# Optimization experiments

Hardware: AMD Instinct MI355X
Metric: run time of the kernel (lower is better)

The kernel has to match this reference:

```python
import jax, jax.numpy as jnp
import numpy as np

B, P, D, A = 256, 196, 512, 512

def setup_inputs() -> dict:
    key = jax.random.key(0)
    ks = jax.random.split(key, 12)
    sc = 1.0 / np.sqrt(D)
    sa = 1.0 / np.sqrt(A)
    return {
        "encoder_out": jax.random.normal(ks[0], (B, P, D), jnp.float32),
        "decoder_hidden": jax.random.normal(ks[1], (B, D), jnp.float32),
        "st": jax.random.normal(ks[2], (B, D), jnp.float32),
        "Wv": jax.random.normal(ks[3], (D, A), jnp.float32) * sc,
        "bv": jnp.zeros((A,), jnp.float32),
        "Wh": jax.random.normal(ks[4], (D, A), jnp.float32) * sc,
        "bh": jnp.zeros((A,), jnp.float32),
        "Ws": jax.random.normal(ks[5], (D, A), jnp.float32) * sc,
        "bs": jnp.zeros((A,), jnp.float32),
        "Wav": jax.random.normal(ks[6], (A,), jnp.float32) * sa,
        "bav": jnp.zeros((), jnp.float32),
        "Was": jax.random.normal(ks[7], (A,), jnp.float32) * sa,
        "bas": jnp.zeros((), jnp.float32),
    }

def reference(encoder_out, decoder_hidden, st, Wv, bv, Wh, bh, Ws, bs, Wav, bav, Was, bas):
    # hidden: (B, A)
    hidden = decoder_hidden @ Wh + bh
    # v: (B, P, A)
    v = jnp.einsum('bpd,da->bpa', encoder_out, Wv) + bv
    # z_t: (B, P) -- additive attention scores over pixels
    z_t = jnp.einsum('bpa,a->bp', jnp.tanh(v + hidden[:, None, :]), Wav) + bav
    alpha_t = jax.nn.softmax(z_t, axis=1)
    # c_t: (B, D) -- attention-weighted encoding
    c_t = jnp.einsum('bpd,bp->bd', encoder_out, alpha_t)
    # sentinel branch: s (B, A), s_att (B, 1)
    s = st @ Ws + bs
    s_att = jnp.tanh(s + hidden) @ Was + bas  # (B,)
    z_t_extended = jnp.concatenate([z_t, s_att[:, None]], axis=1)  # (B, P+1)
    alpha_t_hat = jax.nn.softmax(z_t_extended, axis=1)
    beta_t = alpha_t_hat[:, -1:]  # (B, 1)
    c_hat_t = beta_t * st + (1.0 - beta_t) * c_t
    return (c_hat_t, alpha_t, beta_t)
```

## Files before the change

### kernel.cpp

```cpp
#include <hip/hip_runtime.h>
#include <hip/hip_bf16.h>
#include <cstdint>

#define B_ 256
#define P_ 196
#define D_ 512
#define A_ 512

#define OUT_CHAT  0
#define OUT_ALPHA (B_*D_)
#define OUT_BETA  (B_*D_ + B_*P_)

typedef unsigned short ushort_t;
typedef uint32_t u32;
typedef uint64_t u64;
typedef __attribute__((ext_vector_type(8))) __bf16 bf16x8;
typedef __attribute__((ext_vector_type(4))) float f32x4;

__device__ __forceinline__ ushort_t f2bf(float f) {
    union { float f; u32 i; } v; v.f = f;
    u32 r = (v.i + 0x7fffu + ((v.i >> 16) & 1u)) >> 16;
    return (ushort_t)r;
}
__device__ __forceinline__ float bfbits2f(u32 lo16) {
    union { u32 i; float f; } v; v.i = lo16 << 16; return v.f;
}
__device__ __forceinline__ u32 cvt2bf(float x, float y) {
    union { __hip_bfloat162 h; u32 u; } v;
    v.h = __float22bfloat162_rn(make_float2(x, y));
    return v.u;
}
__device__ __forceinline__ float tanh_fast(float x) {
    float e = __expf(2.0f * x);
    return 1.0f - 2.0f / (e + 1.0f);
}
__device__ __forceinline__ void async_load16(const ushort_t* g, ushort_t* l) {
    __builtin_amdgcn_global_load_lds(
        (const __attribute__((address_space(1))) unsigned int*)g,
        (__attribute__((address_space(3))) unsigned int*)l, 16, 0, 0);
}
__device__ __forceinline__ void fma8(float ap, uint4 v, float ac[8]) {
    ac[0] = fmaf(ap, bfbits2f(v.x & 0xffffu), ac[0]);
    ac[1] = fmaf(ap, bfbits2f(v.x >> 16),     ac[1]);
    ac[2] = fmaf(ap, bfbits2f(v.y & 0xffffu), ac[2]);
    ac[3] = fmaf(ap, bfbits2f(v.y >> 16),     ac[3]);
    ac[4] = fmaf(ap, bfbits2f(v.z & 0xffffu), ac[4]);
    ac[5] = fmaf(ap, bfbits2f(v.z >> 16),     ac[5]);
    ac[6] = fmaf(ap, bfbits2f(v.w & 0xffffu), ac[6]);
    ac[7] = fmaf(ap, bfbits2f(v.w >> 16),     ac[7]);
}

__global__ __launch_bounds__(256) void k_prep(
    const float* __restrict__ E, const float* __restrict__ dh,
    const float* __restrict__ st,
    const float* __restrict__ Wv, const float* __restrict__ Wh,
    const float* __restrict__ Ws,
    ushort_t* __restrict__ Ebf, ushort_t* __restrict__ dhbf,
    ushort_t* __restrict__ stbf,
    ushort_t* __restrict__ WvT, ushort_t* __restrict__ WhT,
    ushort_t* __restrict__ WsT)
{
    __shared__ ushort_t tile[32][33];
    int bx = blockIdx.x;
    if (bx < 12544) {
        size_t i0 = (size_t)bx * 512 + threadIdx.x;
        const float4* src = (const float4*)E;
        u64* dst = (u64*)Ebf;
        float4 v0 = src[i0];
        float4 v1 = src[i0 + 256];
        dst[i0]       = (u64)cvt2bf(v0.x, v0.y) | ((u64)cvt2bf(v0.z, v0.w) << 32);
        dst[i0 + 256] = (u64)cvt2bf(v1.x, v1.y) | ((u64)cvt2bf(v1.z, v1.w) << 32);
    } else if (bx < 12672) {
        int gid = (bx - 12544) * 256 + threadIdx.x;
        float4 dv = ((const float4*)dh)[gid];
        float4 sv = ((const float4*)st)[gid];
        ((u64*)dhbf)[gid] = (u64)cvt2bf(dv.x, dv.y) | ((u64)cvt2bf(dv.z, dv.w) << 32);
        ((u64*)stbf)[gid] = (u64)cvt2bf(sv.x, sv.y) | ((u64)cvt2bf(sv.z, sv.w) << 32);
    } else {
        int idx = bx - 12672;
        int z   = idx >> 8;
        int rem = idx & 255;
        int tby = rem >> 4, tbx = rem & 15;
        const float* W  = (z == 0) ? Wv  : (z == 1) ? Wh  : Ws;
        ushort_t*    WT = (z == 0) ? WvT : (z == 1) ? WhT : WsT;
        int t = threadIdx.x, r = t >> 5, c = t & 31;
#pragma unroll
        for (int i = 0; i < 4; ++i) {
            int row = r + 8 * i;
            tile[row][c] = f2bf(W[(size_t)(tby * 32 + row) * A_ + tbx * 32 + c]);
        }
        __syncthreads();
#pragma unroll
        for (int i = 0; i < 4; ++i) {
            int row = r + 8 * i;
            WT[(size_t)(tbx * 32 + row) * D_ + tby * 32 + c] = tile[c][row];
        }
    }
}

#define PADK 72

__global__ __launch_bounds__(256) void k1_mfma(
    const ushort_t* __restrict__ dhbf, const ushort_t* __restrict__ stbf,
    const ushort_t* __restrict__ WhT,  const ushort_t* __restrict__ WsT,
    const float* __restrict__ bh, const float* __restrict__ bs,
    float* __restrict__ hidden_ws, float* __restrict__ s_ws)
{
    __shared__ ushort_t As[128 * PADK];
    __shared__ ushort_t Bs[128 * PADK];

    int mat = blockIdx.z;
    const ushort_t* Abf = mat ? stbf : dhbf;
    const ushort_t* WT  = mat ? WsT  : WhT;
    const float*    bia = mat ? bs   : bh;
    float*          outp = mat ? s_ws : hidden_ws;

    int tid = threadIdx.x;
    int m0 = blockIdx.y * 128;
    int n0 = blockIdx.x * 128;

    int lane = tid & 63, w = tid >> 6;
    int wm = w & 1, wn = w >> 1;
    int col = lane & 15, q = lane >> 4;

    f32x4 acc[4][4];
#pragma unroll
    for (int tm = 0; tm < 4; ++tm)
#pragma unroll
        for (int tn = 0; tn < 4; ++tn)
            acc[tm][tn] = (f32x4){0.f, 0.f, 0.f, 0.f};

    const ushort_t* arow = As + (wm * 64 + col) * PADK + q * 8;
    const ushort_t* brow = Bs + (wn * 64 + col) * PADK + q * 8;

    int sr = tid >> 3, sc = tid & 7;
    for (int kt = 0; kt < D_ / 64; ++kt) {
#pragma unroll
        for (int i = 0; i < 4; ++i) {
            int row = sr + i * 32;
            *(uint4*)(As + row * PADK + sc * 8) =
                *(const uint4*)(Abf + (size_t)(m0 + row) * D_ + kt * 64 + sc * 8);
            *(uint4*)(Bs + row * PADK + sc * 8) =
                *(const uint4*)(WT + (size_t)(n0 + row) * D_ + kt * 64 + sc * 8);
        }
        __syncthreads();
#pragma unroll
        for (int ks = 0; ks < 2; ++ks) {
            bf16x8 afr[4];
#pragma unroll
            for (int tm = 0; tm < 4; ++tm)
                afr[tm] = *(const bf16x8*)(arow + tm * 16 * PADK + ks * 32);
#pragma unroll
            for (int tn = 0; tn < 4; ++tn) {
                bf16x8 bfr = *(const bf16x8*)(brow + tn * 16 * PADK + ks * 32);
#pragma unroll
                for (int tm = 0; tm < 4; ++tm)
                    acc[tm][tn] = __builtin_amdgcn_mfma_f32_16x16x32_bf16(
                        afr[tm], bfr, acc[tm][tn], 0, 0, 0);
            }
        }
        __syncthreads();
    }

#pragma unroll
    for (int tm = 0; tm < 4; ++tm)
#pragma unroll
        for (int r = 0; r < 4; ++r) {
            int b = m0 + wm * 64 + tm * 16 + q * 4 + r;
#pragma unroll
            for (int tn = 0; tn < 4; ++tn) {
                int n = n0 + wn * 64 + tn * 16 + col;
                outp[(size_t)b * A_ + n] = acc[tm][tn][r] + bia[n];
            }
        }
}

#define BM 128
#define BN2 128
#define BKk 64
__global__ __launch_bounds__(256, 2) void k2_z_bf(
    const ushort_t* __restrict__ Ebf, const ushort_t* __restrict__ WvT,
    const float* __restrict__ hidden_ws, const float* __restrict__ bv,
    const float* __restrict__ Wav, float* __restrict__ z2_ws)
{
    __shared__ ushort_t As[2][BM * BKk];
    __shared__ ushort_t Bs[2][BN2 * BKk];
    __shared__ float hv_s[2][BN2];
    __shared__ float wav_s[BN2];
    __shared__ float zpart[2][BM];

    int tid = threadIdx.x;
    int m0  = blockIdx.x * BM;
    int n0  = blockIdx.y * BN2;
    int b0  = m0 / P_;
    int b1  = (m0 + BM - 1) / P_;

    if (tid < BN2) {
        int a = n0 + tid;
        float bva = bv[a];
        hv_s[0][tid] = hidden_ws[(size_t)b0 * A_ + a] + bva;
        hv_s[1][tid] = hidden_ws[(size_t)b1 * A_ + a] + bva;
        wav_s[tid]   = Wav[a];
    }

    int lane = tid & 63, w = tid >> 6;
    int wm = w & 1, wn = w >> 1;
    int col = lane & 15, q = lane >> 4;

    f32x4 acc[4][4];
#pragma unroll
    for (int tm = 0; tm < 4; ++tm)
#pragma unroll
        for (int tn = 0; tn < 4; ++tn)
            acc[tm][tn] = (f32x4){0.f, 0.f, 0.f, 0.f};

    int srow = tid >> 3, spos = tid & 7;
    int gch  = spos ^ (srow & 7);
    const ushort_t* agb = Ebf + (size_t)(m0 + srow) * D_ + gch * 8;
    const ushort_t* bgb = WvT + (size_t)(n0 + srow) * D_ + gch * 8;

    int fx = col & 7;

#pragma unroll
    for (int i = 0; i < 4; ++i) {
        async_load16(agb + (size_t)i * 32 * D_, &As[0][0] + tid * 8 + i * 2048);
        async_load16(bgb + (size_t)i * 32 * D_, &Bs[0][0] + tid * 8 + i * 2048);
    }
    __syncthreads();

    for (int kt = 0; kt < D_ / BKk; ++kt) {
        int cur = kt & 1;
        if (kt < D_ / BKk - 1) {
#pragma unroll
            for (int i = 0; i < 4; ++i) {
                async_load16(agb + (size_t)i * 32 * D_ + (kt + 1) * BKk,
                             &As[cur ^ 1][0] + tid * 8 + i * 2048);
                async_load16(bgb + (size_t)i * 32 * D_ + (kt + 1) * BKk,
                             &Bs[cur ^ 1][0] + tid * 8 + i * 2048);
            }
        }
        const ushort_t* Ab = &As[cur][0];
        const ushort_t* Bb = &Bs[cur][0];
#pragma unroll
        for (int ks = 0; ks < 2; ++ks) {
            bf16x8 afr[4];
#pragma unroll
            for (int tm = 0; tm < 4; ++tm)
                afr[tm] = *(const bf16x8*)(Ab + (wm * 64 + tm * 16 + col) * BKk
                                              + (((ks * 4 + q) ^ fx) * 8));
#pragma unroll
            for (int tn = 0; tn < 4; ++tn) {
                bf16x8 bfr = *(const bf16x8*)(Bb + (wn * 64 + tn * 16 + col) * BKk
                                                 + (((ks * 4 + q) ^ fx) * 8));
#pragma unroll
                for (int tm = 0; tm < 4; ++tm)
                    acc[tm][tn] = __builtin_amdgcn_mfma_f32_16x16x32_bf16(
                        afr[tm], bfr, acc[tm][tn], 0, 0, 0);
            }
        }
        __syncthreads();
    }

#pragma unroll
    for (int tm = 0; tm < 4; ++tm) {
#pragma unroll
        for (int r = 0; r < 4; ++r) {
            int row = wm * 64 + tm * 16 + q * 4 + r;
            int m   = m0 + row;
            int bsel = (m / P_) - b0;
            float zr = 0.f;
#pragma unroll
            for (int tn = 0; tn < 4; ++tn) {
                int nl = wn * 64 + tn * 16 + col;
                zr += wav_s[nl] * tanh_fast(acc[tm][tn][r] + hv_s[bsel][nl]);
            }
#pragma unroll
            for (int msk = 1; msk < 16; msk <<= 1)
                zr += __shfl_xor(zr, msk, 64);
            if (col == 0) zpart[wn][row] = zr;
        }
    }
    __syncthreads();
    if (tid < BM)
        z2_ws[(size_t)(m0 + tid) * 4 + blockIdx.y] =
            zpart[0][tid] + zpart[1][tid];
}

__global__ __launch_bounds__(512) void k34_softmax_ct(
    const ushort_t* __restrict__ Ebf, const float* __restrict__ st,
    const float* __restrict__ z2_ws, const float* __restrict__ hidden_ws,
    const float* __restrict__ s_ws, const float* __restrict__ Was,
    const float* __restrict__ bas, const float* __restrict__ bav,
    float* __restrict__ out)
{
    __shared__ float red[8];
    __shared__ float al[P_];
    __shared__ float acc_s[8][516];
    __shared__ float bm_s, bl_s, sa_s;

    int b = blockIdx.x, t = threadIdx.x;
    int lane = t & 63, w = t >> 6;

    float part = Was[t] * tanh_fast(s_ws[(size_t)b * A_ + t]
                                  + hidden_ws[(size_t)b * A_ + t]);
#pragma unroll
    for (int o = 32; o >= 1; o >>= 1) part += __shfl_down(part, o, 64);
    if (lane == 0) red[w] = part;
    __syncthreads();
    if (t == 0) {
        float s = 0.f;
#pragma unroll
        for (int i = 0; i < 8; ++i) s += red[i];
        sa_s = s + bas[0];
    }
    __syncthreads();

    float zv = -1e30f;
    if (t < P_) {
        float4 z4 = ((const float4*)z2_ws)[(size_t)b * P_ + t];
        zv = z4.x + z4.y + z4.z + z4.w + bav[0];
    }
    float m = zv;
#pragma unroll
    for (int o = 32; o >= 1; o >>= 1) m = fmaxf(m, __shfl_xor(m, o, 64));
    if (lane == 0) red[w] = m;
    __syncthreads();
    if (t == 0) {
        float mm = red[0];
#pragma unroll
        for (int i = 1; i < 8; ++i) mm = fmaxf(mm, red[i]);
        bm_s = mm;
    }
    __syncthreads();
    float m1 = bm_s;
    float e = (t < P_) ? __expf(zv - m1) : 0.f;
    float s = e;
#pragma unroll
    for (int o = 32; o >= 1; o >>= 1) s += __shfl_xor(s, o, 64);
    if (lane == 0) red[w] = s;
    __syncthreads();
    if (t == 0) {
        float ss = 0.f;
#pragma unroll
        for (int i = 0; i < 8; ++i) ss += red[i];
        bl_s = ss;
    }
    __syncthreads();
    float l1 = bl_s;
    if (t < P_) {
        float alpha = e / l1;
        al[t] = alpha;
        out[OUT_ALPHA + (size_t)b * P_ + t] = alpha;
    }
    float sa = sa_s;
    float m2 = fmaxf(m1, sa);
    float eb2 = __expf(sa - m2);
    float l2 = __expf(m1 - m2) * l1 + eb2;
    float beta = eb2 / l2;
    if (t == 0) out[OUT_BETA + b] = beta;
    __syncthreads();

    float ac[8] = {0.f, 0.f, 0.f, 0.f, 0.f, 0.f, 0.f, 0.f};
    const uint4* eb = (const uint4*)(Ebf + (size_t)b * P_ * D_);
#pragma unroll 4
    for (int i = 0; i < 24; ++i) {
        int pp = w + 8 * i;
        uint4 v = eb[(size_t)pp * (D_ / 8) + lane];
        fma8(al[pp], v, ac);
    }
    if (w < P_ - 192) {
        int pp = 192 + w;
        uint4 v = eb[(size_t)pp * (D_ / 8) + lane];
        fma8(al[pp], v, ac);
    }
#pragma unroll
    for (int j = 0; j < 8; ++j) acc_s[w][lane * 8 + j] = ac[j];
    __syncthreads();
    float c = 0.f;
#pragma unroll
    for (int g = 0; g < 8; ++g) c += acc_s[g][t];
    float sv = st[(size_t)b * D_ + t];
    out[OUT_CHAT + (size_t)b * D_ + t] = beta * sv + (1.f - beta) * c;
}

extern "C" void kernel_launch(void* const* d_in, const int* in_sizes, int n_in,
                              void* d_out, int out_size, void* d_ws, size_t ws_size,
                              hipStream_t stream)
{
    (void)in_sizes; (void)n_in; (void)out_size; (void)ws_size;
    const float* E   = (const float*)d_in[0];
    const float* dh  = (const float*)d_in[1];
    const float* st  = (const float*)d_in[2];
    const float* Wv  = (const float*)d_in[3];
    const float* bv  = (const float*)d_in[4];
    const float* Wh  = (const float*)d_in[5];
    const float* bh  = (const float*)d_in[6];
    const float* Ws  = (const float*)d_in[7];
    const float* bs  = (const float*)d_in[8];
    const float* Wav = (const float*)d_in[9];
    const float* bav = (const float*)d_in[10];
    const float* Was = (const float*)d_in[11];
    const float* bas = (const float*)d_in[12];
    float* out = (float*)d_out;

    char* ws = (char*)d_ws;
    ushort_t* WvT     = (ushort_t*)(ws);
    ushort_t* WhT     = (ushort_t*)(ws + 524288);
    ushort_t* WsT     = (ushort_t*)(ws + 1048576);
    float*    z2_w    = (float*)(ws + 524288);
    ushort_t* dhbf    = (ushort_t*)(ws + 1572864);
    ushort_t* stbf    = (ushort_t*)(ws + 1835008);
    float*    hidden_w= (float*)(ws + 2097152);
    float*    s_w     = (float*)(ws + 2621440);
    ushort_t* Ebf     = (ushort_t*)(ws + 3145728);

    k_prep<<<12544 + 128 + 768, 256, 0, stream>>>(E, dh, st, Wv, Wh, Ws,
                                                  Ebf, dhbf, stbf, WvT, WhT, WsT);
    k1_mfma<<<dim3(4, 2, 2), 256, 0, stream>>>(dhbf, stbf, WhT, WsT, bh, bs,
                                               hidden_w, s_w);
    k2_z_bf<<<dim3((B_ * P_) / BM, A_ / BN2), 256, 0, stream>>>(
        Ebf, WvT, hidden_w, bv, Wav, z2_w);
    k34_softmax_ct<<<256, 512, 0, stream>>>(Ebf, st, z2_w, hidden_w, s_w,
                                            Was, bas, bav, out);
}
```

Before: 256.3 us.

## Deepen k2 GEMM pipeline to four stages with finer K tiles and setprio

```diff
diff --git a/kernel.cpp b/kernel.cpp
--- a/kernel.cpp
+++ b/kernel.cpp
@@ -177,14 +177,14 @@
 
 #define BM 128
 #define BN2 128
-#define BKk 64
+#define BK2 32
 __global__ __launch_bounds__(256, 2) void k2_z_bf(
     const ushort_t* __restrict__ Ebf, const ushort_t* __restrict__ WvT,
     const float* __restrict__ hidden_ws, const float* __restrict__ bv,
     const float* __restrict__ Wav, float* __restrict__ z2_ws)
 {
-    __shared__ ushort_t As[2][BM * BKk];
-    __shared__ ushort_t Bs[2][BN2 * BKk];
+    __shared__ ushort_t As[4][BM * BK2];
+    __shared__ ushort_t Bs[4][BN2 * BK2];
     __shared__ float hv_s[2][BN2];
     __shared__ float wav_s[BN2];
     __shared__ float zpart[2][BM];
@@ -214,52 +214,62 @@
         for (int tn = 0; tn < 4; ++tn)
             acc[tm][tn] = (f32x4){0.f, 0.f, 0.f, 0.f};
 
-    int srow = tid >> 3, spos = tid & 7;
-    int gch  = spos ^ (srow & 7);
-    const ushort_t* agb = Ebf + (size_t)(m0 + srow) * D_ + gch * 8;
-    const ushort_t* bgb = WvT + (size_t)(n0 + srow) * D_ + gch * 8;
-
-    int fx = col & 7;
-
-#pragma unroll
-    for (int i = 0; i < 4; ++i) {
-        async_load16(agb + (size_t)i * 32 * D_, &As[0][0] + tid * 8 + i * 2048);
-        async_load16(bgb + (size_t)i * 32 * D_, &Bs[0][0] + tid * 8 + i * 2048);
-    }
-    __syncthreads();
-
-    for (int kt = 0; kt < D_ / BKk; ++kt) {
-        int cur = kt & 1;
-        if (kt < D_ / BKk - 1) {
-#pragma unroll
-            for (int i = 0; i < 4; ++i) {
-                async_load16(agb + (size_t)i * 32 * D_ + (kt + 1) * BKk,
-                             &As[cur ^ 1][0] + tid * 8 + i * 2048);
-                async_load16(bgb + (size_t)i * 32 * D_ + (kt + 1) * BKk,
-                             &Bs[cur ^ 1][0] + tid * 8 + i * 2048);
-            }
-        }
-        const ushort_t* Ab = &As[cur][0];
-        const ushort_t* Bb = &Bs[cur][0];
-#pragma unroll
-        for (int ks = 0; ks < 2; ++ks) {
-            bf16x8 afr[4];
-#pragma unroll
-            for (int tm = 0; tm < 4; ++tm)
-                afr[tm] = *(const bf16x8*)(Ab + (wm * 64 + tm * 16 + col) * BKk
-                                              + (((ks * 4 + q) ^ fx) * 8));
-#pragma unroll
-            for (int tn = 0; tn < 4; ++tn) {
-                bf16x8 bfr = *(const bf16x8*)(Bb + (wn * 64 + tn * 16 + col) * BKk
-                                                 + (((ks * 4 + q) ^ fx) * 8));
-#pragma unroll
-                for (int tm = 0; tm < 4; ++tm)
-                    acc[tm][tn] = __builtin_amdgcn_mfma_f32_16x16x32_bf16(
-                        afr[tm], bfr, acc[tm][tn], 0, 0, 0);
-            }
-        }
-        __syncthreads();
-    }
+    int gr = w * 32 + (lane >> 2);
+    int gg = (lane & 3) ^ ((lane >> 3) & 3);
+    const ushort_t* agA0 = Ebf + (size_t)(m0 + gr) * D_ + gg * 8;
+    const ushort_t* agA1 = agA0 + (size_t)16 * D_;
+    const ushort_t* agB0 = WvT + (size_t)(n0 + gr) * D_ + gg * 8;
+    const ushort_t* agB1 = agB0 + (size_t)16 * D_;
+    int ldoff = w * 1024 + lane * 8;
+
+#define STAGE(s_) do {                                            \
+    int d_ = (s_) & 3;                                            \
+    int ko_ = (s_) * BK2;                                         \
+    async_load16(agA0 + ko_, &As[d_][0] + ldoff);                 \
+    async_load16(agA1 + ko_, &As[d_][0] + ldoff + 512);           \
+    async_load16(agB0 + ko_, &Bs[d_][0] + ldoff);                 \
+    async_load16(agB1 + ko_, &Bs[d_][0] + ldoff + 512);           \
+} while (0)
+
+    int fx2 = (col >> 1) & 3;
+    int aoff = (wm * 64 + col) * BK2 + ((q ^ fx2) * 8);
+    int boff = (wn * 64 + col) * BK2 + ((q ^ fx2) * 8);
+
+#define COMPUTE(kt_) do {                                         \
+    const ushort_t* Ab_ = &As[(kt_) & 3][0];                      \
+    const ushort_t* Bb_ = &Bs[(kt_) & 3][0];                      \
+    bf16x8 afr_[4];                                               \
+    _Pragma("unroll")                                             \
+    for (int tm = 0; tm < 4; ++tm)                                \
+        afr_[tm] = *(const bf16x8*)(Ab_ + aoff + tm * 512);       \
+    __builtin_amdgcn_s_setprio(1);                                \
+    _Pragma("unroll")                                             \
+    for (int tn = 0; tn < 4; ++tn) {                              \
+        bf16x8 bfr_ = *(const bf16x8*)(Bb_ + boff + tn * 512);    \
+        _Pragma("unroll")                                         \
+        for (int tm = 0; tm < 4; ++tm)                            \
+            acc[tm][tn] = __builtin_amdgcn_mfma_f32_16x16x32_bf16(\
+                afr_[tm], bfr_, acc[tm][tn], 0, 0, 0);            \
+    }                                                             \
+    __builtin_amdgcn_s_setprio(0);                                \
+} while (0)
+
+    STAGE(0); STAGE(1); STAGE(2);
+    for (int kt = 0; kt < 14; ++kt) {
+        asm volatile("s_waitcnt vmcnt(8)" ::: "memory");
+        __builtin_amdgcn_s_barrier();
+        if (kt < 13) STAGE(kt + 3);
+        COMPUTE(kt);
+    }
+    asm volatile("s_waitcnt vmcnt(4)" ::: "memory");
+    __builtin_amdgcn_s_barrier();
+    COMPUTE(14);
+    asm volatile("s_waitcnt vmcnt(0)" ::: "memory");
+    __builtin_amdgcn_s_barrier();
+    COMPUTE(15);
+
+#undef STAGE
+#undef COMPUTE
 
 #pragma unroll
     for (int tm = 0; tm < 4; ++tm) {
```

After: 262.2 us. 2.3% more time.

## Prefetch two K-tiles ahead with explicit vmcnt waits and MFMA priority

Applied to the files above, without the earlier changes.

```diff
diff --git a/kernel.cpp b/kernel.cpp
--- a/kernel.cpp
+++ b/kernel.cpp
@@ -221,45 +221,59 @@
 
     int fx = col & 7;
 
-#pragma unroll
-    for (int i = 0; i < 4; ++i) {
-        async_load16(agb + (size_t)i * 32 * D_, &As[0][0] + tid * 8 + i * 2048);
-        async_load16(bgb + (size_t)i * 32 * D_, &Bs[0][0] + tid * 8 + i * 2048);
-    }
-    __syncthreads();
-
+#define STAGE(buf_, kt_) do {                                           \
+    _Pragma("unroll")                                                   \
+    for (int i = 0; i < 4; ++i) {                                       \
+        async_load16(agb + (size_t)i * 32 * D_ + (kt_) * BKk,           \
+                     &As[buf_][0] + tid * 8 + i * 2048);                \
+        async_load16(bgb + (size_t)i * 32 * D_ + (kt_) * BKk,           \
+                     &Bs[buf_][0] + tid * 8 + i * 2048);                \
+    }                                                                   \
+} while (0)
+
+#define COMPUTE(cur_) do {                                              \
+    const ushort_t* Ab_ = &As[cur_][0];                                 \
+    const ushort_t* Bb_ = &Bs[cur_][0];                                 \
+    __builtin_amdgcn_s_setprio(1);                                      \
+    _Pragma("unroll")                                                   \
+    for (int ks = 0; ks < 2; ++ks) {                                    \
+        bf16x8 afr_[4];                                                 \
+        _Pragma("unroll")                                               \
+        for (int tm = 0; tm < 4; ++tm)                                  \
+            afr_[tm] = *(const bf16x8*)(Ab_                             \
+                + (wm * 64 + tm * 16 + col) * BKk                       \
+                + (((ks * 4 + q) ^ fx) * 8));                           \
+        _Pragma("unroll")                                               \
+        for (int tn = 0; tn < 4; ++tn) {                                \
+            bf16x8 bfr_ = *(const bf16x8*)(Bb_                          \
+                + (wn * 64 + tn * 16 + col) * BKk                       \
+                + (((ks * 4 + q) ^ fx) * 8));                           \
+            _Pragma("unroll")                                           \
+            for (int tm = 0; tm < 4; ++tm)                              \
+                acc[tm][tn] = __builtin_amdgcn_mfma_f32_16x16x32_bf16(  \
+                    afr_[tm], bfr_, acc[tm][tn], 0, 0, 0);              \
+        }                                                               \
+    }                                                                   \
+    __builtin_amdgcn_s_setprio(0);                                      \
+} while (0)
+
+    STAGE(0, 0);
+    STAGE(1, 1);
+#pragma unroll
     for (int kt = 0; kt < D_ / BKk; ++kt) {
-        int cur = kt & 1;
-        if (kt < D_ / BKk - 1) {
-#pragma unroll
-            for (int i = 0; i < 4; ++i) {
-                async_load16(agb + (size_t)i * 32 * D_ + (kt + 1) * BKk,
-                             &As[cur ^ 1][0] + tid * 8 + i * 2048);
-                async_load16(bgb + (size_t)i * 32 * D_ + (kt + 1) * BKk,
-                             &Bs[cur ^ 1][0] + tid * 8 + i * 2048);
-            }
-        }
-        const ushort_t* Ab = &As[cur][0];
-        const ushort_t* Bb = &Bs[cur][0];
-#pragma unroll
-        for (int ks = 0; ks < 2; ++ks) {
-            bf16x8 afr[4];
-#pragma unroll
-            for (int tm = 0; tm < 4; ++tm)
-                afr[tm] = *(const bf16x8*)(Ab + (wm * 64 + tm * 16 + col) * BKk
-                                              + (((ks * 4 + q) ^ fx) * 8));
-#pragma unroll
-            for (int tn = 0; tn < 4; ++tn) {
-                bf16x8 bfr = *(const bf16x8*)(Bb + (wn * 64 + tn * 16 + col) * BKk
-                                                 + (((ks * 4 + q) ^ fx) * 8));
-#pragma unroll
-                for (int tm = 0; tm < 4; ++tm)
-                    acc[tm][tn] = __builtin_amdgcn_mfma_f32_16x16x32_bf16(
-                        afr[tm], bfr, acc[tm][tn], 0, 0, 0);
-            }
-        }
-        __syncthreads();
-    }
+        if (kt < D_ / BKk - 1)
+            asm volatile("s_waitcnt vmcnt(8)" ::: "memory");
+        else
+            asm volatile("s_waitcnt vmcnt(0)" ::: "memory");
+        __builtin_amdgcn_s_barrier();
+        COMPUTE(kt & 1);
+        __builtin_amdgcn_s_barrier();
+        if (kt < D_ / BKk - 2)
+            STAGE(kt & 1, kt + 2);
+    }
+
+#undef STAGE
+#undef COMPUTE
 
 #pragma unroll
     for (int tm = 0; tm < 4; ++tm) {
```

New measurement: 255.9 us. No clear change (-0.1%).
